# Optimization experiments

Measured on AMD Instinct MI355X. Metric: run time of the kernel, lower is better.

Reference implementation:

```python
import jax, jax.numpy as jnp
import numpy as np

B, L, D, H, DFF = 4, 2048, 1024, 16, 4096
DH = D // H
INF = 1e12


def setup_inputs() -> dict:
    key = jax.random.key(0)
    ks = jax.random.split(key, 20)
    s = lambda fan_in: 1.0 / np.sqrt(fan_in)
    inp = {
        'x': jax.random.normal(ks[0], (B, L, D), jnp.float32),
        'mask': jax.random.bernoulli(ks[1], 0.1, (B, 1, 1, L)),
        'wq': jax.random.normal(ks[2], (D, D), jnp.float32) * s(D),
        'bq': jnp.zeros((D,), jnp.float32),
        'wk': jax.random.normal(ks[3], (D, D), jnp.float32) * s(D),
        'bk': jnp.zeros((D,), jnp.float32),
        'wv': jax.random.normal(ks[4], (D, D), jnp.float32) * s(D),
        'bv': jnp.zeros((D,), jnp.float32),
        'wo': jax.random.normal(ks[5], (D, D), jnp.float32) * s(D),
        'bo': jnp.zeros((D,), jnp.float32),
        'w1': jax.random.normal(ks[6], (D, DFF), jnp.float32) * s(D),
        'b1': jnp.zeros((DFF,), jnp.float32),
        'w2': jax.random.normal(ks[7], (DFF, D), jnp.float32) * s(DFF),
        'b2': jnp.zeros((D,), jnp.float32),
        'g1': jnp.ones((D,), jnp.float32),
        'beta1': jnp.zeros((D,), jnp.float32),
        'g2': jnp.ones((D,), jnp.float32),
        'beta2': jnp.zeros((D,), jnp.float32),
    }
    return inp


def _layernorm(x, g, b, eps=1e-5):
    mu = jnp.mean(x, axis=-1, keepdims=True)
    var = jnp.mean(jnp.square(x - mu), axis=-1, keepdims=True)
    return (x - mu) * jax.lax.rsqrt(var + eps) * g + b


def reference(x, mask, wq, bq, wk, bk, wv, bv, wo, bo, w1, b1, w2, b2, g1, beta1, g2, beta2):
    # --- self attention ---
    def split_heads(t):  # [B,L,D] -> [B,H,L,DH]
        return t.reshape(B, L, H, DH).transpose(0, 2, 1, 3)

    Q = split_heads(x @ wq + bq)
    K = split_heads(x @ wk + bk)
    V = split_heads(x @ wv + bv)

    dots = jnp.einsum('bhqd,bhkd->bhqk', Q, K) / np.sqrt(DH)  # [B,H,L,L]
    dots = jnp.where(mask, -INF, dots)
    attn = jax.nn.softmax(dots, axis=-1)
    out = jnp.einsum('bhqk,bhkd->bhqd', attn, V)
    out = out.transpose(0, 2, 1, 3).reshape(B, L, D)
    out = out @ wo + bo

    x = _layernorm(x + out, g1, beta1)

    # --- feed forward ---
    h = jax.nn.relu(x @ w1 + b1)
    ff = h @ w2 + b2
    x = _layernorm(x + ff, g2, beta2)
    return x
```

## Files before the change

kernel.cpp:

```cpp
#include <hip/hip_runtime.h>
#include <hip/hip_bf16.h>

#define B_   4
#define L_   2048
#define D_   1024
#define H_   16
#define DH_  64
#define DFF_ 4096
#define M_   (B_ * L_)

typedef __attribute__((ext_vector_type(8))) short bf16x8;
typedef __attribute__((ext_vector_type(4))) float f32x4;

#define GLOAD16(gp, lp)                                                       \
  __builtin_amdgcn_global_load_lds(                                           \
      (const __attribute__((address_space(1))) unsigned int*)(gp),            \
      (__attribute__((address_space(3))) unsigned int*)(lp), 16, 0, 0)

#if __has_builtin(__builtin_amdgcn_exp2f)
#define EXP2F(x) __builtin_amdgcn_exp2f(x)
#else
#define EXP2F(x) exp2f(x)
#endif

__global__ void mask_mode_detect(const unsigned int* __restrict__ m,
                                 int* __restrict__ mode) {
  __shared__ int flags[2];
  if (threadIdx.x < 2) flags[threadIdx.x] = 0;
  __syncthreads();
  int nf32 = 0, n01 = 0;
  for (int i = threadIdx.x; i < 2048; i += 256) {
    unsigned w = m[i];
    if (w != 0u && w != 0x3f800000u) nf32 = 1;
    if (w > 1u) n01 = 1;
  }
  if (nf32) atomicOr(&flags[0], 1);
  if (n01)  atomicOr(&flags[1], 1);
  __syncthreads();
  if (threadIdx.x == 0)
    *mode = (!flags[0]) ? 0 : ((!flags[1]) ? 1 : 2);
}

__global__ void mask_prep(const void* __restrict__ m,
                          const int* __restrict__ mode_p,
                          float* __restrict__ out, int n) {
  int i = blockIdx.x * 256 + threadIdx.x;
  if (i >= n) return;
  int mode = *mode_p;
  bool mk;
  if (mode == 0)      mk = reinterpret_cast<const float*>(m)[i] != 0.f;
  else if (mode == 1) mk = reinterpret_cast<const int*>(m)[i] != 0;
  else                mk = reinterpret_cast<const unsigned char*>(m)[i] != 0;
  out[i] = mk ? -1e12f : 0.f;
}

__global__ void cvt_f32_bf16(const float4* __restrict__ in,
                             ushort4* __restrict__ out, int n4) {
  int i = blockIdx.x * 256 + threadIdx.x;
  if (i >= n4) return;
  float4 v = in[i];
  __hip_bfloat16 a = __float2bfloat16(v.x);
  __hip_bfloat16 b = __float2bfloat16(v.y);
  __hip_bfloat16 c = __float2bfloat16(v.z);
  __hip_bfloat16 d = __float2bfloat16(v.w);
  ushort4 o;
  o.x = *reinterpret_cast<unsigned short*>(&a);
  o.y = *reinterpret_cast<unsigned short*>(&b);
  o.z = *reinterpret_cast<unsigned short*>(&c);
  o.w = *reinterpret_cast<unsigned short*>(&d);
  out[i] = o;
}

__global__ void transpose_cvt(const float* __restrict__ W,
                              __hip_bfloat16* __restrict__ Wt, int K, int N) {
  __shared__ float t[32][33];
  const int n0 = blockIdx.x * 32, k0 = blockIdx.y * 32;
  const int tx = threadIdx.x, ty = threadIdx.y;
#pragma unroll
  for (int i = 0; i < 4; ++i)
    t[ty + i * 8][tx] = W[(size_t)(k0 + ty + i * 8) * N + n0 + tx];
  __syncthreads();
#pragma unroll
  for (int i = 0; i < 4; ++i)
    Wt[(size_t)(n0 + ty + i * 8) * K + k0 + tx] =
        __float2bfloat16(t[tx][ty + i * 8]);
}

__global__ void transpose_v(const __hip_bfloat16* __restrict__ Vin,
                            __hip_bfloat16* __restrict__ Vt) {
  __shared__ __hip_bfloat16 t[32][33];
  const int l0 = blockIdx.x * 32, d0 = blockIdx.y * 32, b = blockIdx.z;
  const int tx = threadIdx.x, ty = threadIdx.y;
#pragma unroll
  for (int i = 0; i < 4; ++i)
    t[ty + i * 8][tx] = Vin[(size_t)(b * L_ + l0 + ty + i * 8) * D_ + d0 + tx];
  __syncthreads();
#pragma unroll
  for (int i = 0; i < 4; ++i) {
    int d = d0 + ty + i * 8;
    Vt[(size_t)(b * D_ + d) * L_ + l0 + tx] = t[tx][ty + i * 8];
  }
}

#define STAGE8(matptr, stride, ldsbase, tile, kh, rowbase)                    \
  {                                                                           \
    _Pragma("unroll")                                                         \
    for (int j_ = 0; j_ < 2; ++j_) {                                          \
      const int s_ = j_ * 512 + tid;                                          \
      const int row_ = s_ >> 2;                                               \
// ... 99 lines not shown
  __builtin_amdgcn_s_barrier();

  for (int it = 0; it < nit; ++it) {
    const int kt = it * 2;
    const bool hn = (it + 1) < nit;
    PHASE8(0, 0, 0, 0, STAGE8(Ap, lda, ldsA + 49152, kt + 1, 1, bm));
    PHASE8(0, 1, 0, 0, STAGE8(Bp, ldb, ldsB + 49152, kt + 1, 1, bn));
    PHASE8(0, 0, 1, 0, if (hn) STAGE8(Ap, lda, ldsA, kt + 2, 0, bm));
    PHASE8(0, 1, 1, 1, if (hn) STAGE8(Bp, ldb, ldsB, kt + 2, 0, bn));
    PHASE8(32768, 0, 0, 0, if (hn) STAGE8(Ap, lda, ldsA + 16384, kt + 2, 1, bm));
    PHASE8(32768, 1, 0, 0, if (hn) STAGE8(Bp, ldb, ldsB + 16384, kt + 2, 1, bn));
    PHASE8(32768, 0, 1, 0, if (hn) STAGE8(Ap, lda, ldsA + 32768, kt + 3, 0, bm));
    PHASE8(32768, 1, 1, 1, if (hn) STAGE8(Bp, ldb, ldsB + 32768, kt + 3, 0, bn));
  }

#pragma unroll
  for (int ri = 0; ri < 8; ++ri) {
#pragma unroll
    for (int j = 0; j < 4; ++j) {
      const int col = bn + wn * 64 + j * 16 + r16;
      const float bv = (EP == 4) ? 0.f : bias[col];
#pragma unroll
      for (int r = 0; r < 4; ++r) {
        const int row = bm + wm * 128 + ri * 16 + hi * 4 + r;
        const float v = acc[ri][j][r] + bv;
        if (EP == 1) {
          ((__hip_bfloat16*)out)[(size_t)row * N + col] =
              __float2bfloat16(v > 0.f ? v : 0.f);
        } else if (EP == 3) {
          __hip_bfloat16* outp =
              (__hip_bfloat16*)out + (size_t)(col >> 10) * (M_ * D_);
          outp[(size_t)row * 1024 + (col & 1023)] = __float2bfloat16(v);
        } else {
          float* outp = (float*)out + (size_t)kh * ((size_t)M * N);
          outp[(size_t)row * N + col] = v;
        }
      }
    }
  }
}

template <int EP>
__global__ __launch_bounds__(256) void gemm_bt(
    const __hip_bfloat16* __restrict__ A, const __hip_bfloat16* __restrict__ Bt,
    const float* __restrict__ bias, const float* __restrict__ res,
    void* __restrict__ out, int M, int N, int K) {
  __shared__ __align__(16) char As[128 * 64];
  __shared__ __align__(16) char Bs[128 * 64];
  const int tid = threadIdx.x;
  const int lane = tid & 63;
  const int w = tid >> 6;
  const int wm = w >> 1, wn = w & 1;
  const int bm = blockIdx.x * 128;
  const int bn = blockIdx.y * 128;
  const int r16 = lane & 15;
  const int hi = lane >> 4;

  f32x4 acc[4][4];
#pragma unroll
  for (int m = 0; m < 4; ++m)
#pragma unroll
    for (int n = 0; n < 4; ++n) acc[m][n] = (f32x4){0.f, 0.f, 0.f, 0.f};

  for (int k0 = 0; k0 < K; k0 += 32) {
    __syncthreads();
#pragma unroll
    for (int c = 0; c < 2; ++c) {
      const int seg = c * 256 + tid;
// ... 11 lines not shown
    for (int m = 0; m < 4; ++m) {
      const int arow = wm * 64 + m * 16 + r16;
      af[m] = *reinterpret_cast<const bf16x8*>(
          As + arow * 64 + ((hi * 16) ^ ((arow & 3) << 4)));
    }
#pragma unroll
    for (int n = 0; n < 4; ++n) {
      const int brow = wn * 64 + n * 16 + r16;
      bfr[n] = *reinterpret_cast<const bf16x8*>(
          Bs + brow * 64 + ((hi * 16) ^ ((brow & 3) << 4)));
    }
#pragma unroll
    for (int m = 0; m < 4; ++m)
#pragma unroll
      for (int n = 0; n < 4; ++n)
        acc[m][n] = __builtin_amdgcn_mfma_f32_16x16x32_bf16(af[m], bfr[n],
                                                            acc[m][n], 0, 0, 0);
  }

  const int rg = hi * 4;
#pragma unroll
  for (int m = 0; m < 4; ++m) {
#pragma unroll
    for (int n = 0; n < 4; ++n) {
      const int col = bn + wn * 64 + n * 16 + r16;
      const float bv = bias[col];
#pragma unroll
      for (int r = 0; r < 4; ++r) {
        const int row = bm + wm * 64 + m * 16 + rg + r;
        const size_t idx = (size_t)row * N + col;
        float v = acc[m][n][r] + bv;
        if (EP == 0) {
          ((__hip_bfloat16*)out)[idx] = __float2bfloat16(v);
        } else if (EP == 1) {
          ((__hip_bfloat16*)out)[idx] = __float2bfloat16(v > 0.f ? v : 0.f);
        } else {
          ((float*)out)[idx] = v + res[idx];
        }
      }
    }
  }
}

__global__ __launch_bounds__(256) void attn_kernel(
    const __hip_bfloat16* __restrict__ Qg, const __hip_bfloat16* __restrict__ Kg,
    const __hip_bfloat16* __restrict__ VTg,
    const float* __restrict__ maskf,
    __hip_bfloat16* __restrict__ Og) {
  __shared__ __align__(16) char Kl[64 * 128];
  __shared__ __align__(16) char Vl[64 * 128];
  __shared__ __align__(16) char Pl[4][32 * 128];
  __shared__ float maskb[64];

  const int tid = threadIdx.x;
  const int lane = tid & 63;
  const int w = tid >> 6;
  const int hi = lane >> 4;
  const int r16 = lane & 15;
  const int swzk = (r16 & 7) << 4;

  const int nwg = gridDim.x;
  const int orig = blockIdx.x;
  const int swb = (orig & 7) * (nwg >> 3) + (orig >> 3);
  const int qb = swb & 15;
  const int bh = swb >> 4;
  const int b = bh >> 4;
  const int h = bh & 15;
  const int qbase = qb * 128 + w * 32;

  const float C = 0.18033688011112042f;

  bf16x8 qf[2][2];
#pragma unroll
  for (int m = 0; m < 2; ++m)
#pragma unroll
    for (int ks = 0; ks < 2; ++ks)
      qf[m][ks] = *reinterpret_cast<const bf16x8*>(
          &Qg[(size_t)(b * L_ + qbase + m * 16 + r16) * D_ + h * DH_ +
              ks * 32 + hi * 8]);

  float mrun[2] = {-1e30f, -1e30f};
  float lrun[2] = {0.f, 0.f};
  f32x4 o[2][4];
#pragma unroll
  for (int m = 0; m < 2; ++m)
#pragma unroll
    for (int nd = 0; nd < 4; ++nd) o[m][nd] = (f32x4){0.f, 0.f, 0.f, 0.f};

  char* const Plw = Pl[w];

  for (int kv0 = 0; kv0 < L_; kv0 += 64) {
    __syncthreads();
#pragma unroll
    for (int c = 0; c < 2; ++c) {
      const int seg = c * 256 + tid;
      const int row = seg >> 3;
      const int csl = (seg & 7) ^ (row & 7);
      GLOAD16(&Kg[(size_t)(b * L_ + kv0 + row) * D_ + h * DH_ + csl * 8],
              Kl + (c * 256 + w * 64) * 16);
      GLOAD16(&VTg[(size_t)(b * D_ + h * DH_ + row) * L_ + kv0 + csl * 8],
              Vl + (c * 256 + w * 64) * 16);
    }
    if (tid < 64) maskb[tid] = maskf[(size_t)b * L_ + kv0 + tid];
    __syncthreads();

    f32x4 sacc[2][4];
#pragma unroll
    for (int m = 0; m < 2; ++m)
#pragma unroll
      for (int n = 0; n < 4; ++n) sacc[m][n] = (f32x4){0.f, 0.f, 0.f, 0.f};
    __builtin_amdgcn_s_setprio(1);
#pragma unroll
    for (int n = 0; n < 4; ++n) {
      const int krow = n * 16 + r16;
#pragma unroll
      for (int ks = 0; ks < 2; ++ks) {
        const bf16x8 kf = *reinterpret_cast<const bf16x8*>(
            Kl + krow * 128 + ((ks * 64 + hi * 16) ^ swzk));
#pragma unroll
        for (int m = 0; m < 2; ++m)
          sacc[m][n] = __builtin_amdgcn_mfma_f32_16x16x32_bf16(
              kf, qf[m][ks], sacc[m][n], 0, 0, 0);
      }
    }
    __builtin_amdgcn_s_setprio(0);

#pragma unroll
    for (int m = 0; m < 2; ++m) {
      float p[4][4];
#pragma unroll
      for (int n = 0; n < 4; ++n) {
        const float4 mv =
            *reinterpret_cast<const float4*>(&maskb[n * 16 + hi * 4]);
        p[n][0] = fmaf(sacc[m][n][0], C, mv.x);
        p[n][1] = fmaf(sacc[m][n][1], C, mv.y);
        p[n][2] = fmaf(sacc[m][n][2], C, mv.z);
        p[n][3] = fmaf(sacc[m][n][3], C, mv.w);
      }
      float q0 = fmaxf(fmaxf(p[0][0], p[0][1]), fmaxf(p[0][2], p[0][3]));
      float q1 = fmaxf(fmaxf(p[1][0], p[1][1]), fmaxf(p[1][2], p[1][3]));
      float q2 = fmaxf(fmaxf(p[2][0], p[2][1]), fmaxf(p[2][2], p[2][3]));
      float q3 = fmaxf(fmaxf(p[3][0], p[3][1]), fmaxf(p[3][2], p[3][3]));
      float lm = fmaxf(fmaxf(q0, q1), fmaxf(q2, q3));
      lm = fmaxf(lm, __shfl_xor(lm, 16, 64));
      lm = fmaxf(lm, __shfl_xor(lm, 32, 64));
      if (!__all(lm <= mrun[m] + 8.f)) {
        const float mn = fmaxf(mrun[m], lm);
        const float corr = EXP2F(mrun[m] - mn);
        mrun[m] = mn;
        lrun[m] *= corr;
        float crs[4];
#pragma unroll
        for (int r = 0; r < 4; ++r)
          crs[r] = __shfl(corr, (lane & 48) | (hi * 4 + r), 64);
#pragma unroll
        for (int nd = 0; nd < 4; ++nd)
#pragma unroll
          for (int r = 0; r < 4; ++r) o[m][nd][r] *= crs[r];
      }
      const float mr = mrun[m];
      float ls = 0.f;
      const int prow = m * 16 + r16;
#pragma unroll
      for (int n = 0; n < 4; ++n) {
        union { unsigned long long u; unsigned short us[4]; } pk;
#pragma unroll
        for (int r = 0; r < 4; ++r) {
          const float e = EXP2F(p[n][r] - mr);
          ls += e;
          __hip_bfloat16 t = __float2bfloat16(e);
          pk.us[r] = *reinterpret_cast<unsigned short*>(&t);
        }
        *reinterpret_cast<unsigned long long*>(
            Plw + prow * 128 + ((n * 32 + hi * 8) ^ swzk)) = pk.u;
      }
      lrun[m] += ls;
    }

    bf16x8 pa[2][2];
#pragma unroll
    for (int m = 0; m < 2; ++m)
#pragma unroll
      for (int ks = 0; ks < 2; ++ks)
        pa[m][ks] = *reinterpret_cast<const bf16x8*>(
            Plw + (m * 16 + r16) * 128 + ((ks * 64 + hi * 16) ^ swzk));
    __builtin_amdgcn_s_setprio(1);
#pragma unroll
    for (int nd = 0; nd < 4; ++nd) {
      const int vrow = nd * 16 + r16;
#pragma unroll
      for (int ks = 0; ks < 2; ++ks) {
        const bf16x8 vb = *reinterpret_cast<const bf16x8*>(
            Vl + vrow * 128 + ((ks * 64 + hi * 16) ^ swzk));
#pragma unroll
        for (int m = 0; m < 2; ++m)
          o[m][nd] = __builtin_amdgcn_mfma_f32_16x16x32_bf16(pa[m][ks], vb,
                                                             o[m][nd], 0, 0, 0);
      }
    }
    __builtin_amdgcn_s_setprio(0);
  }

#pragma unroll
  for (int m = 0; m < 2; ++m) {
    lrun[m] += __shfl_xor(lrun[m], 16, 64);
    lrun[m] += __shfl_xor(lrun[m], 32, 64);
    const float inv = 1.f / lrun[m];
    float invr[4];
#pragma unroll
    for (int r = 0; r < 4; ++r)
      invr[r] = __shfl(inv, (lane & 48) | (hi * 4 + r), 64);
#pragma unroll
    for (int r = 0; r < 4; ++r) {
      const int q = qbase + m * 16 + hi * 4 + r;
#pragma unroll
      for (int nd = 0; nd < 4; ++nd)
        Og[(size_t)(b * L_ + q) * D_ + h * DH_ + nd * 16 + r16] =
            __float2bfloat16(o[m][nd][r] * invr[r]);
    }
  }
}

__global__ __launch_bounds__(256) void layernorm_kernel(
    const float* __restrict__ in, const float* __restrict__ g,
    const float* __restrict__ be, float* __restrict__ outf,
    __hip_bfloat16* __restrict__ outb) {
  const int row = blockIdx.x;
  const int tid = threadIdx.x;
  const float4 v = reinterpret_cast<const float4*>(in + (size_t)row * D_)[tid];
  float s = v.x + v.y + v.z + v.w;
  float ss = v.x * v.x + v.y * v.y + v.z * v.z + v.w * v.w;
#pragma unroll
  for (int off = 1; off < 64; off <<= 1) {
    s += __shfl_xor(s, off, 64);
    ss += __shfl_xor(ss, off, 64);
  }
  __shared__ float red[8];
  const int w = tid >> 6, lane = tid & 63;
  if (lane == 0) { red[w] = s; red[4 + w] = ss; }
  __syncthreads();
  s = red[0] + red[1] + red[2] + red[3];
  ss = red[4] + red[5] + red[6] + red[7];
  const float mu = s * (1.f / D_);
  const float rs = rsqrtf(ss * (1.f / D_) - mu * mu + 1e-5f);
  const float4 gv = reinterpret_cast<const float4*>(g)[tid];
  const float4 bv = reinterpret_cast<const float4*>(be)[tid];
  float4 ov;
  ov.x = (v.x - mu) * rs * gv.x + bv.x;
  ov.y = (v.y - mu) * rs * gv.y + bv.y;
  ov.z = (v.z - mu) * rs * gv.z + bv.z;
  ov.w = (v.w - mu) * rs * gv.w + bv.w;
  reinterpret_cast<float4*>(outf + (size_t)row * D_)[tid] = ov;
  if (outb) {
    __hip_bfloat16 t[4] = {__float2bfloat16(ov.x), __float2bfloat16(ov.y),
                           __float2bfloat16(ov.z), __float2bfloat16(ov.w)};
    *reinterpret_cast<uint2*>(&outb[(size_t)row * D_ + tid * 4]) =
        *reinterpret_cast<const uint2*>(t);
  }
}

__global__ __launch_bounds__(256) void combine_ln2(
    const float* __restrict__ P0, const float* __restrict__ P1,
    const float* __restrict__ res, const float* __restrict__ b2,
    const float* __restrict__ g, const float* __restrict__ be,
    float* __restrict__ out) {
  const int row = blockIdx.x;
  const int tid = threadIdx.x;
  const float4 a = reinterpret_cast<const float4*>(P0 + (size_t)row * D_)[tid];
  const float4 b = reinterpret_cast<const float4*>(P1 + (size_t)row * D_)[tid];
  const float4 rr = reinterpret_cast<const float4*>(res + (size_t)row * D_)[tid];
  const float4 bb = reinterpret_cast<const float4*>(b2)[tid];
  float4 v;
  v.x = a.x + b.x + rr.x + bb.x;
  v.y = a.y + b.y + rr.y + bb.y;
  v.z = a.z + b.z + rr.z + bb.z;
  v.w = a.w + b.w + rr.w + bb.w;
  float s = v.x + v.y + v.z + v.w;
  float ss = v.x * v.x + v.y * v.y + v.z * v.z + v.w * v.w;
#pragma unroll
  for (int off = 1; off < 64; off <<= 1) {
    s += __shfl_xor(s, off, 64);
    ss += __shfl_xor(ss, off, 64);
  }
  __shared__ float red[8];
  const int w = tid >> 6, lane = tid & 63;
  if (lane == 0) { red[w] = s; red[4 + w] = ss; }
  __syncthreads();
  s = red[0] + red[1] + red[2] + red[3];
  ss = red[4] + red[5] + red[6] + red[7];
  const float mu = s * (1.f / D_);
  const float rs = rsqrtf(ss * (1.f / D_) - mu * mu + 1e-5f);
  const float4 gv = reinterpret_cast<const float4*>(g)[tid];
  const float4 bv = reinterpret_cast<const float4*>(be)[tid];
  float4 ov;
  ov.x = (v.x - mu) * rs * gv.x + bv.x;
  ov.y = (v.y - mu) * rs * gv.y + bv.y;
  ov.z = (v.z - mu) * rs * gv.z + bv.z;
  ov.w = (v.w - mu) * rs * gv.w + bv.w;
  reinterpret_cast<float4*>(out + (size_t)row * D_)[tid] = ov;
}

extern "C" void kernel_launch(void* const* d_in, const int* in_sizes, int n_in,
                              void* d_out, int out_size, void* d_ws,
                              size_t ws_size, hipStream_t stream) {
  (void)in_sizes; (void)n_in; (void)out_size;
  const float* x   = (const float*)d_in[0];
  const void*  msk = d_in[1];
  const float* wq  = (const float*)d_in[2];
  const float* bq  = (const float*)d_in[3];
  const float* wk  = (const float*)d_in[4];
  const float* bk  = (const float*)d_in[5];
  const float* wv  = (const float*)d_in[6];
  const float* bv  = (const float*)d_in[7];
  const float* wo  = (const float*)d_in[8];
  const float* bo  = (const float*)d_in[9];
  const float* w1  = (const float*)d_in[10];
  const float* b1  = (const float*)d_in[11];
  const float* w2  = (const float*)d_in[12];
  const float* b2  = (const float*)d_in[13];
  const float* g1  = (const float*)d_in[14];
  const float* be1 = (const float*)d_in[15];
  const float* g2  = (const float*)d_in[16];
  const float* be2 = (const float*)d_in[17];

  char* ws = (char*)d_ws;
  int*            MODE  = (int*)(ws + 0);
  float*          MASKF = (float*)(ws + 256);
  float*          BIASC = (float*)(ws + 40960);
  __hip_bfloat16* XB    = (__hip_bfloat16*)(ws + 65536);
  __hip_bfloat16* WQT   = (__hip_bfloat16*)(ws + 16842752);
  __hip_bfloat16* WKT   = (__hip_bfloat16*)(ws + 18939904);
  __hip_bfloat16* WVT   = (__hip_bfloat16*)(ws + 21037056);
  __hip_bfloat16* WOT   = (__hip_bfloat16*)(ws + 23134208);
  __hip_bfloat16* W1T   = (__hip_bfloat16*)(ws + 25231360);
  __hip_bfloat16* W2T   = (__hip_bfloat16*)(ws + 33619968);
  __hip_bfloat16* QB    = (__hip_bfloat16*)(ws + 42008576);
  __hip_bfloat16* KB    = (__hip_bfloat16*)(ws + 58785792);
  __hip_bfloat16* VB    = (__hip_bfloat16*)(ws + 75563008);
  __hip_bfloat16* OB    = (__hip_bfloat16*)(ws + 92340224);
  __hip_bfloat16* HB    = QB;
  __hip_bfloat16* VT    = (__hip_bfloat16*)(ws + 109117440);
  float*          R1    = (float*)(ws + 125894656);
  float*          P0    = (float*)(ws + 159449088);
  float*          P1    = (float*)(ws + 193003520);
  float*          OUT   = (float*)d_out;
  const bool use_splitk = ws_size >= 226557952ull;

  mask_mode_detect<<<1, 256, 0, stream>>>((const unsigned int*)msk, MODE);
  mask_prep<<<(B_ * L_ + 255) / 256, 256, 0, stream>>>(msk, MODE, MASKF, B_ * L_);
  cvt_f32_bf16<<<(M_ * D_ / 4 + 255) / 256, 256, 0, stream>>>(
      (const float4*)x, (ushort4*)XB, M_ * D_ / 4);
  hipMemcpyAsync(BIASC, bq, D_ * 4, hipMemcpyDeviceToDevice, stream);
  hipMemcpyAsync(BIASC + D_, bk, D_ * 4, hipMemcpyDeviceToDevice, stream);
  hipMemcpyAsync(BIASC + 2 * D_, bv, D_ * 4, hipMemcpyDeviceToDevice, stream);

  dim3 tb(32, 8);
  transpose_cvt<<<dim3(D_ / 32, D_ / 32), tb, 0, stream>>>(wq, WQT, D_, D_);
  transpose_cvt<<<dim3(D_ / 32, D_ / 32), tb, 0, stream>>>(wk, WKT, D_, D_);
  transpose_cvt<<<dim3(D_ / 32, D_ / 32), tb, 0, stream>>>(wv, WVT, D_, D_);
  transpose_cvt<<<dim3(D_ / 32, D_ / 32), tb, 0, stream>>>(wo, WOT, D_, D_);
  transpose_cvt<<<dim3(DFF_ / 32, D_ / 32), tb, 0, stream>>>(w1, W1T, D_, DFF_);
  transpose_cvt<<<dim3(D_ / 32, DFF_ / 32), tb, 0, stream>>>(w2, W2T, DFF_, D_);

  gemm8<3><<<dim3((M_ / 256) * (3 * D_ / 256)), 512, 0, stream>>>(
      XB, WQT, BIASC, QB, M_, 3 * D_, D_, D_, D_);

  transpose_v<<<dim3(L_ / 32, D_ / 32, B_), tb, 0, stream>>>(VB, VT);
  attn_kernel<<<dim3(B_ * H_ * (L_ / 128)), 256, 0, stream>>>(QB, KB, VT, MASKF, OB);

  gemm_bt<2><<<dim3(M_ / 128, D_ / 128), 256, 0, stream>>>(OB, WOT, bo, x, R1, M_, D_, D_);
  layernorm_kernel<<<M_, 256, 0, stream>>>(R1, g1, be1, R1, XB);
  gemm8<1><<<dim3((M_ / 256) * (DFF_ / 256)), 512, 0, stream>>>(
      XB, W1T, b1, HB, M_, DFF_, D_, D_, D_);
  if (use_splitk) {
    gemm8<4><<<dim3((M_ / 256) * (D_ / 256) * 2), 512, 0, stream>>>(
        HB, W2T, nullptr, P0, M_, D_, DFF_ / 2, DFF_, DFF_);
    combine_ln2<<<M_, 256, 0, stream>>>(P0, P1, R1, b2, g2, be2, OUT);
  } else {
    gemm_bt<2><<<dim3(M_ / 128, D_ / 128), 256, 0, stream>>>(HB, W2T, b2, R1, OUT, M_, D_, DFF_);
    layernorm_kernel<<<M_, 256, 0, stream>>>(OUT, g2, be2, OUT, nullptr);
  }
}
```

Baseline: 474.3 us.

## Prefetch next K/V tiles in attention loop and store split-K partials as bf16

The attention kernel now issues the global-to-LDS loads for the next K tile after the QK MFMAs, and for the next V tile after the PV MFMAs. It double-buffers the mask and uses vmcnt waits with explicit barriers, so memory latency overlaps with compute instead of stalling at the top of each iteration. Separately, the split-K FFN2 partial sums are written as bf16 instead of fp32, and combine_ln2 reads them back as bf16. This halves the partial-buffer traffic and workspace size but adds rounding error to the pre-layernorm sum.

```diff
diff --git a/kernel.cpp b/kernel.cpp
--- a/kernel.cpp
+++ b/kernel.cpp
@@ -22,6 +22,10 @@
 #else
 #define EXP2F(x) exp2f(x)
 #endif
+
+__device__ __forceinline__ float bf2f(unsigned short u) {
+  return __uint_as_float(((unsigned)u) << 16);
+}
 
 __global__ void mask_mode_detect(const unsigned int* __restrict__ m,
                                  int* __restrict__ mode) {
@@ -240,8 +244,9 @@
               (__hip_bfloat16*)out + (size_t)(col >> 10) * (M_ * D_);
           outp[(size_t)row * 1024 + (col & 1023)] = __float2bfloat16(v);
         } else {
-          float* outp = (float*)out + (size_t)kh * ((size_t)M * N);
-          outp[(size_t)row * N + col] = v;
+          __hip_bfloat16* outp =
+              (__hip_bfloat16*)out + (size_t)kh * ((size_t)M * N);
+          outp[(size_t)row * N + col] = __float2bfloat16(v);
         }
       }
     }
@@ -337,7 +342,7 @@
   __shared__ __align__(16) char Kl[64 * 128];
   __shared__ __align__(16) char Vl[64 * 128];
   __shared__ __align__(16) char Pl[4][32 * 128];
-  __shared__ float maskb[64];
+  __shared__ float maskb[2][64];
 
   const int tid = threadIdx.x;
   const int lane = tid & 63;
@@ -357,6 +362,27 @@
 
   const float C = 0.18033688011112042f;
 
+#define STAGE_K(kvv)                                                          \
+  {                                                                           \
+    _Pragma("unroll") for (int c_ = 0; c_ < 2; ++c_) {                        \
+      const int seg_ = c_ * 256 + tid;                                        \
+      const int row_ = seg_ >> 3;                                             \
+      const int csl_ = (seg_ & 7) ^ (row_ & 7);                               \
+      GLOAD16(&Kg[(size_t)(b * L_ + (kvv) + row_) * D_ + h * DH_ + csl_ * 8], \
+              Kl + (c_ * 256 + w * 64) * 16);                                 \
+    }                                                                         \
+  }
+#define STAGE_V(kvv)                                                          \
+  {                                                                           \
+    _Pragma("unroll") for (int c_ = 0; c_ < 2; ++c_) {                        \
+      const int seg_ = c_ * 256 + tid;                                        \
+      const int row_ = seg_ >> 3;                                             \
+      const int csl_ = (seg_ & 7) ^ (row_ & 7);                               \
+      GLOAD16(&VTg[(size_t)(b * D_ + h * DH_ + row_) * L_ + (kvv) + csl_ * 8],\
+              Vl + (c_ * 256 + w * 64) * 16);                                 \
+    }                                                                         \
+  }
+
   bf16x8 qf[2][2];
 #pragma unroll
   for (int m = 0; m < 2; ++m)
@@ -376,20 +402,19 @@
 
   char* const Plw = Pl[w];
 
-  for (int kv0 = 0; kv0 < L_; kv0 += 64) {
-    __syncthreads();
-#pragma unroll
-    for (int c = 0; c < 2; ++c) {
-      const int seg = c * 256 + tid;
-      const int row = seg >> 3;
-      const int csl = (seg & 7) ^ (row & 7);
-      GLOAD16(&Kg[(size_t)(b * L_ + kv0 + row) * D_ + h * DH_ + csl * 8],
-              Kl + (c * 256 + w * 64) * 16);
-      GLOAD16(&VTg[(size_t)(b * D_ + h * DH_ + row) * L_ + kv0 + csl * 8],
-              Vl + (c * 256 + w * 64) * 16);
-    }
-    if (tid < 64) maskb[tid] = maskf[(size_t)b * L_ + kv0 + tid];
-    __syncthreads();
+  STAGE_K(0);
+  float mreg = 0.f;
+  if (tid < 64) mreg = maskf[(size_t)b * L_ + tid];
+  STAGE_V(0);
+  if (tid < 64) maskb[0][tid] = mreg;
+  asm volatile("s_waitcnt vmcnt(2)" ::: "memory");
+  __builtin_amdgcn_sched_barrier(0);
+  __builtin_amdgcn_s_barrier();
+  __builtin_amdgcn_sched_barrier(0);
+
+  for (int t = 0; t < 32; ++t) {
+    const int slot = t & 1;
+    const int kvn = ((t + 1) & 31) * 64;
 
     f32x4 sacc[2][4];
 #pragma unroll
@@ -411,6 +436,9 @@
       }
     }
     __builtin_amdgcn_s_setprio(0);
+    __builtin_amdgcn_s_barrier();
+    __builtin_amdgcn_sched_barrier(0);
+    STAGE_K(kvn);
 
 #pragma unroll
     for (int m = 0; m < 2; ++m) {
@@ -418,7 +446,7 @@
 #pragma unroll
       for (int n = 0; n < 4; ++n) {
         const float4 mv =
-            *reinterpret_cast<const float4*>(&maskb[n * 16 + hi * 4]);
+            *reinterpret_cast<const float4*>(&maskb[slot][n * 16 + hi * 4]);
         p[n][0] = fmaf(sacc[m][n][0], C, mv.x);
         p[n][1] = fmaf(sacc[m][n][1], C, mv.y);
         p[n][2] = fmaf(sacc[m][n][2], C, mv.z);
@@ -455,8 +483,8 @@
         for (int r = 0; r < 4; ++r) {
           const float e = EXP2F(p[n][r] - mr);
           ls += e;
-          __hip_bfloat16 t = __float2bfloat16(e);
-          pk.us[r] = *reinterpret_cast<unsigned short*>(&t);
+          __hip_bfloat16 tt = __float2bfloat16(e);
+          pk.us[r] = *reinterpret_cast<unsigned short*>(&tt);
         }
         *reinterpret_cast<unsigned long long*>(
             Plw + prow * 128 + ((n * 32 + hi * 8) ^ swzk)) = pk.u;
@@ -464,6 +492,11 @@
       lrun[m] += ls;
     }
 
+    asm volatile("s_waitcnt vmcnt(2)" ::: "memory");
+    __builtin_amdgcn_sched_barrier(0);
+    __builtin_amdgcn_s_barrier();
+    __builtin_amdgcn_sched_barrier(0);
+
     bf16x8 pa[2][2];
 #pragma unroll
     for (int m = 0; m < 2; ++m)
@@ -486,6 +519,16 @@
       }
     }
     __builtin_amdgcn_s_setprio(0);
+    __builtin_amdgcn_s_barrier();
+    __builtin_amdgcn_sched_barrier(0);
+
+    if (tid < 64) mreg = maskf[(size_t)b * L_ + kvn + tid];
+    STAGE_V(kvn);
+    if (tid < 64) maskb[slot ^ 1][tid] = mreg;
+    asm volatile("s_waitcnt vmcnt(2)" ::: "memory");
+    __builtin_amdgcn_sched_barrier(0);
+    __builtin_amdgcn_s_barrier();
+    __builtin_amdgcn_sched_barrier(0);
   }
 
 #pragma unroll
@@ -506,6 +549,8 @@
             __float2bfloat16(o[m][nd][r] * invr[r]);
     }
   }
+#undef STAGE_K
+#undef STAGE_V
 }
 
 __global__ __launch_bounds__(256) void layernorm_kernel(
@@ -547,21 +592,23 @@
 }
 
 __global__ __launch_bounds__(256) void combine_ln2(
-    const float* __restrict__ P0, const float* __restrict__ P1,
+    const __hip_bfloat16* __restrict__ P0, const __hip_bfloat16* __restrict__ P1,
     const float* __restrict__ res, const float* __restrict__ b2,
     const float* __restrict__ g, const float* __restrict__ be,
     float* __restrict__ out) {
   const int row = blockIdx.x;
   const int tid = threadIdx.x;
-  const float4 a = reinterpret_cast<const float4*>(P0 + (size_t)row * D_)[tid];
-  const float4 b = reinterpret_cast<const float4*>(P1 + (size_t)row * D_)[tid];
+  const ushort4 a4 =
+      reinterpret_cast<const ushort4*>(P0 + (size_t)row * D_)[tid];
+  const ushort4 b4 =
+      reinterpret_cast<const ushort4*>(P1 + (size_t)row * D_)[tid];
   const float4 rr = reinterpret_cast<const float4*>(res + (size_t)row * D_)[tid];
   const float4 bb = reinterpret_cast<const float4*>(b2)[tid];
   float4 v;
-  v.x = a.x + b.x + rr.x + bb.x;
-  v.y = a.y + b.y + rr.y + bb.y;
-  v.z = a.z + b.z + rr.z + bb.z;
-  v.w = a.w + b.w + rr.w + bb.w;
+  v.x = bf2f(a4.x) + bf2f(b4.x) + rr.x + bb.x;
+  v.y = bf2f(a4.y) + bf2f(b4.y) + rr.y + bb.y;
+  v.z = bf2f(a4.z) + bf2f(b4.z) + rr.z + bb.z;
+  v.w = bf2f(a4.w) + bf2f(b4.w) + rr.w + bb.w;
   float s = v.x + v.y + v.z + v.w;
   float ss = v.x * v.x + v.y * v.y + v.z * v.z + v.w * v.w;
 #pragma unroll
@@ -628,10 +675,10 @@
   __hip_bfloat16* HB    = QB;
   __hip_bfloat16* VT    = (__hip_bfloat16*)(ws + 109117440);
   float*          R1    = (float*)(ws + 125894656);
-  float*          P0    = (float*)(ws + 159449088);
-  float*          P1    = (float*)(ws + 193003520);
+  __hip_bfloat16* P0    = (__hip_bfloat16*)(ws + 159449088);
+  __hip_bfloat16* P1    = (__hip_bfloat16*)(ws + 176226304);
   float*          OUT   = (float*)d_out;
-  const bool use_splitk = ws_size >= 226557952ull;
+  const bool use_splitk = ws_size >= 193003520ull;
 
   mask_mode_detect<<<1, 256, 0, stream>>>((const unsigned int*)msk, MODE);
   mask_prep<<<(B_ * L_ + 255) / 256, 256, 0, stream>>>(msk, MODE, MASKF, B_ * L_);
```

Result: faster. 463.6 us (-2.3%).

## Use 32x32 MFMA with register-resident P in attention; bf16 split-K partials

Applied to the files above, without the earlier changes.

The attention kernel moves from 16x16x32 to 32x32x16 bf16 MFMA tiles with one 32-row query block per wave. The softmax probabilities are packed to bf16 in registers and exchanged across half-waves with shuffles instead of a round trip through per-wave LDS, which removes the P shared buffer. Separately, the split-K FFN2 partials are stored as bf16 rather than fp32 and the combine/LayerNorm kernel reads bf16, halving that traffic at some precision cost. The workspace threshold for enabling split-K is lowered to match the smaller buffers.

```diff
diff --git a/kernel.cpp b/kernel.cpp
--- a/kernel.cpp
+++ b/kernel.cpp
@@ -11,6 +11,7 @@
 
 typedef __attribute__((ext_vector_type(8))) short bf16x8;
 typedef __attribute__((ext_vector_type(4))) float f32x4;
+typedef __attribute__((ext_vector_type(16))) float f32x16;
 
 #define GLOAD16(gp, lp)                                                       \
   __builtin_amdgcn_global_load_lds(                                           \
@@ -22,6 +23,15 @@
 #else
 #define EXP2F(x) exp2f(x)
 #endif
+
+__device__ __forceinline__ float bf2f(unsigned short u) {
+  return __uint_as_float(((unsigned)u) << 16);
+}
+__device__ __forceinline__ unsigned cvt_pk_bf16(float lo, float hi) {
+  unsigned r;
+  asm("v_cvt_pk_bf16_f32 %0, %1, %2" : "=v"(r) : "v"(lo), "v"(hi));
+  return r;
+}
 
 __global__ void mask_mode_detect(const unsigned int* __restrict__ m,
                                  int* __restrict__ mode) {
@@ -240,8 +250,9 @@
               (__hip_bfloat16*)out + (size_t)(col >> 10) * (M_ * D_);
           outp[(size_t)row * 1024 + (col & 1023)] = __float2bfloat16(v);
         } else {
-          float* outp = (float*)out + (size_t)kh * ((size_t)M * N);
-          outp[(size_t)row * N + col] = v;
+          __hip_bfloat16* outp =
+              (__hip_bfloat16*)out + (size_t)kh * ((size_t)M * N);
+          outp[(size_t)row * N + col] = __float2bfloat16(v);
         }
       }
     }
@@ -336,15 +347,13 @@
     __hip_bfloat16* __restrict__ Og) {
   __shared__ __align__(16) char Kl[64 * 128];
   __shared__ __align__(16) char Vl[64 * 128];
-  __shared__ __align__(16) char Pl[4][32 * 128];
   __shared__ float maskb[64];
 
   const int tid = threadIdx.x;
   const int lane = tid & 63;
   const int w = tid >> 6;
-  const int hi = lane >> 4;
-  const int r16 = lane & 15;
-  const int swzk = (r16 & 7) << 4;
+  const int l31 = lane & 31;
+  const int h5 = lane >> 5;
 
   const int nwg = gridDim.x;
   const int orig = blockIdx.x;
@@ -357,24 +366,19 @@
 
   const float C = 0.18033688011112042f;
 
-  bf16x8 qf[2][2];
-#pragma unroll
-  for (int m = 0; m < 2; ++m)
-#pragma unroll
-    for (int ks = 0; ks < 2; ++ks)
-      qf[m][ks] = *reinterpret_cast<const bf16x8*>(
-          &Qg[(size_t)(b * L_ + qbase + m * 16 + r16) * D_ + h * DH_ +
-              ks * 32 + hi * 8]);
-
-  float mrun[2] = {-1e30f, -1e30f};
-  float lrun[2] = {0.f, 0.f};
-  f32x4 o[2][4];
-#pragma unroll
-  for (int m = 0; m < 2; ++m)
-#pragma unroll
-    for (int nd = 0; nd < 4; ++nd) o[m][nd] = (f32x4){0.f, 0.f, 0.f, 0.f};
-
-  char* const Plw = Pl[w];
+  bf16x8 qf[4];
+#pragma unroll
+  for (int dk = 0; dk < 4; ++dk)
+    qf[dk] = *reinterpret_cast<const bf16x8*>(
+        &Qg[(size_t)(b * L_ + qbase + l31) * D_ + h * DH_ + dk * 16 + h5 * 8]);
+
+  float mrun = -1e30f;
+  float lrun = 0.f;
+  f32x16 o[2];
+#pragma unroll
+  for (int nd = 0; nd < 2; ++nd)
+#pragma unroll
+    for (int r = 0; r < 16; ++r) o[nd][r] = 0.f;
 
   for (int kv0 = 0; kv0 < L_; kv0 += 64) {
     __syncthreads();
@@ -391,120 +395,122 @@
     if (tid < 64) maskb[tid] = maskf[(size_t)b * L_ + kv0 + tid];
     __syncthreads();
 
-    f32x4 sacc[2][4];
-#pragma unroll
-    for (int m = 0; m < 2; ++m)
-#pragma unroll
-      for (int n = 0; n < 4; ++n) sacc[m][n] = (f32x4){0.f, 0.f, 0.f, 0.f};
+    f32x16 sac[2];
+#pragma unroll
+    for (int n = 0; n < 2; ++n)
+#pragma unroll
+      for (int r = 0; r < 16; ++r) sac[n][r] = 0.f;
     __builtin_amdgcn_s_setprio(1);
 #pragma unroll
-    for (int n = 0; n < 4; ++n) {
-      const int krow = n * 16 + r16;
-#pragma unroll
-      for (int ks = 0; ks < 2; ++ks) {
+    for (int n = 0; n < 2; ++n) {
+      const int krow = n * 32 + l31;
+      const int rsw = (krow & 7) << 4;
+#pragma unroll
+      for (int dk = 0; dk < 4; ++dk) {
         const bf16x8 kf = *reinterpret_cast<const bf16x8*>(
-            Kl + krow * 128 + ((ks * 64 + hi * 16) ^ swzk));
-#pragma unroll
-        for (int m = 0; m < 2; ++m)
-          sacc[m][n] = __builtin_amdgcn_mfma_f32_16x16x32_bf16(
-              kf, qf[m][ks], sacc[m][n], 0, 0, 0);
+            Kl + krow * 128 + ((dk * 32 + h5 * 16) ^ rsw));
+        sac[n] = __builtin_amdgcn_mfma_f32_32x32x16_bf16(kf, qf[dk], sac[n],
+                                                         0, 0, 0);
       }
     }
     __builtin_amdgcn_s_setprio(0);
 
 #pragma unroll
-    for (int m = 0; m < 2; ++m) {
-      float p[4][4];
-#pragma unroll
-      for (int n = 0; n < 4; ++n) {
-        const float4 mv =
-            *reinterpret_cast<const float4*>(&maskb[n * 16 + hi * 4]);
-        p[n][0] = fmaf(sacc[m][n][0], C, mv.x);
-        p[n][1] = fmaf(sacc[m][n][1], C, mv.y);
-        p[n][2] = fmaf(sacc[m][n][2], C, mv.z);
-        p[n][3] = fmaf(sacc[m][n][3], C, mv.w);
+    for (int n = 0; n < 2; ++n)
+#pragma unroll
+      for (int q_ = 0; q_ < 4; ++q_) {
+        const float4 mv = *reinterpret_cast<const float4*>(
+            &maskb[n * 32 + q_ * 8 + h5 * 4]);
+        sac[n][q_ * 4 + 0] = fmaf(sac[n][q_ * 4 + 0], C, mv.x);
+        sac[n][q_ * 4 + 1] = fmaf(sac[n][q_ * 4 + 1], C, mv.y);
+        sac[n][q_ * 4 + 2] = fmaf(sac[n][q_ * 4 + 2], C, mv.z);
+        sac[n][q_ * 4 + 3] = fmaf(sac[n][q_ * 4 + 3], C, mv.w);
       }
-      float q0 = fmaxf(fmaxf(p[0][0], p[0][1]), fmaxf(p[0][2], p[0][3]));
-      float q1 = fmaxf(fmaxf(p[1][0], p[1][1]), fmaxf(p[1][2], p[1][3]));
-      float q2 = fmaxf(fmaxf(p[2][0], p[2][1]), fmaxf(p[2][2], p[2][3]));
-      float q3 = fmaxf(fmaxf(p[3][0], p[3][1]), fmaxf(p[3][2], p[3][3]));
-      float lm = fmaxf(fmaxf(q0, q1), fmaxf(q2, q3));
-      lm = fmaxf(lm, __shfl_xor(lm, 16, 64));
-      lm = fmaxf(lm, __shfl_xor(lm, 32, 64));
-      if (!__all(lm <= mrun[m] + 8.f)) {
-        const float mn = fmaxf(mrun[m], lm);
-        const float corr = EXP2F(mrun[m] - mn);
-        mrun[m] = mn;
-        lrun[m] *= corr;
-        float crs[4];
-#pragma unroll
-        for (int r = 0; r < 4; ++r)
-          crs[r] = __shfl(corr, (lane & 48) | (hi * 4 + r), 64);
-#pragma unroll
-        for (int nd = 0; nd < 4; ++nd)
-#pragma unroll
-          for (int r = 0; r < 4; ++r) o[m][nd][r] *= crs[r];
+
+    float lm = sac[0][0];
+#pragma unroll
+    for (int n = 0; n < 2; ++n)
+#pragma unroll
+      for (int r = 0; r < 16; ++r) lm = fmaxf(lm, sac[n][r]);
+    lm = fmaxf(lm, __shfl_xor(lm, 32, 64));
+
+    if (!__all(lm <= mrun + 8.f)) {
+      const float mn = fmaxf(mrun, lm);
+      const float corr = EXP2F(mrun - mn);
+      mrun = mn;
+      lrun *= corr;
+#pragma unroll
+      for (int r = 0; r < 16; ++r) {
+        const int ql = (r & 3) + 8 * (r >> 2) + 4 * h5;
+        const float cr = __shfl(corr, ql, 64);
+        o[0][r] *= cr;
+        o[1][r] *= cr;
       }
-      const float mr = mrun[m];
-      float ls = 0.f;
-      const int prow = m * 16 + r16;
-#pragma unroll
-      for (int n = 0; n < 4; ++n) {
-        union { unsigned long long u; unsigned short us[4]; } pk;
-#pragma unroll
-        for (int r = 0; r < 4; ++r) {
-          const float e = EXP2F(p[n][r] - mr);
-          ls += e;
-          __hip_bfloat16 t = __float2bfloat16(e);
-          pk.us[r] = *reinterpret_cast<unsigned short*>(&t);
-        }
-        *reinterpret_cast<unsigned long long*>(
-            Plw + prow * 128 + ((n * 32 + hi * 8) ^ swzk)) = pk.u;
+    }
+
+    const float mr = mrun;
+    float ls = 0.f;
+    unsigned pp[2][4][2];
+#pragma unroll
+    for (int n = 0; n < 2; ++n)
+#pragma unroll
+      for (int q_ = 0; q_ < 4; ++q_) {
+        float e0 = EXP2F(sac[n][q_ * 4 + 0] - mr);
+        float e1 = EXP2F(sac[n][q_ * 4 + 1] - mr);
+        float e2 = EXP2F(sac[n][q_ * 4 + 2] - mr);
+        float e3 = EXP2F(sac[n][q_ * 4 + 3] - mr);
+        ls += (e0 + e1) + (e2 + e3);
+        pp[n][q_][0] = cvt_pk_bf16(e0, e1);
+        pp[n][q_][1] = cvt_pk_bf16(e2, e3);
       }
-      lrun[m] += ls;
-    }
-
-    bf16x8 pa[2][2];
-#pragma unroll
-    for (int m = 0; m < 2; ++m)
-#pragma unroll
-      for (int ks = 0; ks < 2; ++ks)
-        pa[m][ks] = *reinterpret_cast<const bf16x8*>(
-            Plw + (m * 16 + r16) * 128 + ((ks * 64 + hi * 16) ^ swzk));
+    lrun += ls;
+
+    bf16x8 pa[4];
+#pragma unroll
+    for (int kb = 0; kb < 4; ++kb) {
+      const int n = kb >> 1;
+      const int qe = (kb & 1) * 2;
+      const unsigned oe0 = pp[n][qe][0], oe1 = pp[n][qe][1];
+      const unsigned oo0 = pp[n][qe + 1][0], oo1 = pp[n][qe + 1][1];
+      const unsigned xe0 = __shfl_xor(oe0, 32, 64);
+      const unsigned xe1 = __shfl_xor(oe1, 32, 64);
+      const unsigned xo0 = __shfl_xor(oo0, 32, 64);
+      const unsigned xo1 = __shfl_xor(oo1, 32, 64);
+      union { unsigned u[4]; bf16x8 v; } pu;
+      pu.u[0] = h5 ? xo0 : oe0;
+      pu.u[1] = h5 ? xo1 : oe1;
+      pu.u[2] = h5 ? oo0 : xe0;
+      pu.u[3] = h5 ? oo1 : xe1;
+      pa[kb] = pu.v;
+    }
+
     __builtin_amdgcn_s_setprio(1);
 #pragma unroll
-    for (int nd = 0; nd < 4; ++nd) {
-      const int vrow = nd * 16 + r16;
-#pragma unroll
-      for (int ks = 0; ks < 2; ++ks) {
+    for (int nd = 0; nd < 2; ++nd) {
+      const int vrow = nd * 32 + l31;
+      const int rsw = (vrow & 7) << 4;
+#pragma unroll
+      for (int kb = 0; kb < 4; ++kb) {
         const bf16x8 vb = *reinterpret_cast<const bf16x8*>(
-            Vl + vrow * 128 + ((ks * 64 + hi * 16) ^ swzk));
-#pragma unroll
-        for (int m = 0; m < 2; ++m)
-          o[m][nd] = __builtin_amdgcn_mfma_f32_16x16x32_bf16(pa[m][ks], vb,
-                                                             o[m][nd], 0, 0, 0);
+            Vl + vrow * 128 + ((kb * 32 + h5 * 16) ^ rsw));
+        o[nd] = __builtin_amdgcn_mfma_f32_32x32x16_bf16(pa[kb], vb, o[nd],
+                                                        0, 0, 0);
       }
     }
     __builtin_amdgcn_s_setprio(0);
   }
 
-#pragma unroll
-  for (int m = 0; m < 2; ++m) {
-    lrun[m] += __shfl_xor(lrun[m], 16, 64);
-    lrun[m] += __shfl_xor(lrun[m], 32, 64);
-    const float inv = 1.f / lrun[m];
-    float invr[4];
-#pragma unroll
-    for (int r = 0; r < 4; ++r)
-      invr[r] = __shfl(inv, (lane & 48) | (hi * 4 + r), 64);
-#pragma unroll
-    for (int r = 0; r < 4; ++r) {
-      const int q = qbase + m * 16 + hi * 4 + r;
-#pragma unroll
-      for (int nd = 0; nd < 4; ++nd)
-        Og[(size_t)(b * L_ + q) * D_ + h * DH_ + nd * 16 + r16] =
-            __float2bfloat16(o[m][nd][r] * invr[r]);
-    }
+  lrun += __shfl_xor(lrun, 32, 64);
+  const float inv = 1.f / lrun;
+#pragma unroll
+  for (int r = 0; r < 16; ++r) {
+    const int ql = (r & 3) + 8 * (r >> 2) + 4 * h5;
+    const float ir = __shfl(inv, ql, 64);
+    const int q = qbase + ql;
+#pragma unroll
+    for (int nd = 0; nd < 2; ++nd)
+      Og[(size_t)(b * L_ + q) * D_ + h * DH_ + nd * 32 + l31] =
+          __float2bfloat16(o[nd][r] * ir);
   }
 }
 
@@ -547,21 +553,23 @@
 }
 
 __global__ __launch_bounds__(256) void combine_ln2(
-    const float* __restrict__ P0, const float* __restrict__ P1,
+    const __hip_bfloat16* __restrict__ P0, const __hip_bfloat16* __restrict__ P1,
     const float* __restrict__ res, const float* __restrict__ b2,
     const float* __restrict__ g, const float* __restrict__ be,
     float* __restrict__ out) {
   const int row = blockIdx.x;
   const int tid = threadIdx.x;
-  const float4 a = reinterpret_cast<const float4*>(P0 + (size_t)row * D_)[tid];
-  const float4 b = reinterpret_cast<const float4*>(P1 + (size_t)row * D_)[tid];
+  const ushort4 a4 =
+      reinterpret_cast<const ushort4*>(P0 + (size_t)row * D_)[tid];
+  const ushort4 b4 =
+      reinterpret_cast<const ushort4*>(P1 + (size_t)row * D_)[tid];
   const float4 rr = reinterpret_cast<const float4*>(res + (size_t)row * D_)[tid];
   const float4 bb = reinterpret_cast<const float4*>(b2)[tid];
   float4 v;
-  v.x = a.x + b.x + rr.x + bb.x;
-  v.y = a.y + b.y + rr.y + bb.y;
-  v.z = a.z + b.z + rr.z + bb.z;
-  v.w = a.w + b.w + rr.w + bb.w;
+  v.x = bf2f(a4.x) + bf2f(b4.x) + rr.x + bb.x;
+  v.y = bf2f(a4.y) + bf2f(b4.y) + rr.y + bb.y;
+  v.z = bf2f(a4.z) + bf2f(b4.z) + rr.z + bb.z;
+  v.w = bf2f(a4.w) + bf2f(b4.w) + rr.w + bb.w;
   float s = v.x + v.y + v.z + v.w;
   float ss = v.x * v.x + v.y * v.y + v.z * v.z + v.w * v.w;
 #pragma unroll
@@ -628,10 +636,10 @@
   __hip_bfloat16* HB    = QB;
   __hip_bfloat16* VT    = (__hip_bfloat16*)(ws + 109117440);
   float*          R1    = (float*)(ws + 125894656);
-  float*          P0    = (float*)(ws + 159449088);
-  float*          P1    = (float*)(ws + 193003520);
+  __hip_bfloat16* P0    = (__hip_bfloat16*)(ws + 159449088);
+  __hip_bfloat16* P1    = (__hip_bfloat16*)(ws + 176226304);
   float*          OUT   = (float*)d_out;
-  const bool use_splitk = ws_size >= 226557952ull;
+  const bool use_splitk = ws_size >= 193003520ull;
 
   mask_mode_detect<<<1, 256, 0, stream>>>((const unsigned int*)msk, MODE);
   mask_prep<<<(B_ * L_ + 255) / 256, 256, 0, stream>>>(msk, MODE, MASKF, B_ * L_);
```

New measurement: 467.7 us. No clear change (-1.4%).

## Merge prep kernels, batch weight transposes, and store GEMM partials in bf16

Applied to the files above, without the earlier changes.

Mask-mode detection, mask preparation and bias concatenation now run in one kernel, and the six weight transpose launches become a single launch. The output projection now writes bf16 with no residual, and the residual add moves into a new layernorm kernel. The split-K FFN2 partials are stored as bf16 instead of fp32. This cuts launch count and global memory traffic, at the cost of extra rounding error in the partial sums and projection output.

```diff
diff --git a/kernel.cpp b/kernel.cpp
--- a/kernel.cpp
+++ b/kernel.cpp
@@ -23,35 +23,46 @@
 #define EXP2F(x) exp2f(x)
 #endif
 
-__global__ void mask_mode_detect(const unsigned int* __restrict__ m,
-                                 int* __restrict__ mode) {
+__device__ __forceinline__ float bf2f(unsigned short u) {
+  return __uint_as_float(((unsigned)u) << 16);
+}
+
+__global__ void prep_kernel(const unsigned int* __restrict__ mraw,
+                            float* __restrict__ maskf,
+                            const float* __restrict__ bq,
+                            const float* __restrict__ bk,
+                            const float* __restrict__ bv,
+                            float* __restrict__ biasc) {
   __shared__ int flags[2];
   if (threadIdx.x < 2) flags[threadIdx.x] = 0;
   __syncthreads();
   int nf32 = 0, n01 = 0;
   for (int i = threadIdx.x; i < 2048; i += 256) {
-    unsigned w = m[i];
+    unsigned w = mraw[i];
     if (w != 0u && w != 0x3f800000u) nf32 = 1;
     if (w > 1u) n01 = 1;
   }
   if (nf32) atomicOr(&flags[0], 1);
   if (n01)  atomicOr(&flags[1], 1);
   __syncthreads();
-  if (threadIdx.x == 0)
-    *mode = (!flags[0]) ? 0 : ((!flags[1]) ? 1 : 2);
-}
-
-__global__ void mask_prep(const void* __restrict__ m,
-                          const int* __restrict__ mode_p,
-                          float* __restrict__ out, int n) {
-  int i = blockIdx.x * 256 + threadIdx.x;
-  if (i >= n) return;
-  int mode = *mode_p;
-  bool mk;
-  if (mode == 0)      mk = reinterpret_cast<const float*>(m)[i] != 0.f;
-  else if (mode == 1) mk = reinterpret_cast<const int*>(m)[i] != 0;
-  else                mk = reinterpret_cast<const unsigned char*>(m)[i] != 0;
-  out[i] = mk ? -1e12f : 0.f;
+  const int mode = (!flags[0]) ? 0 : ((!flags[1]) ? 1 : 2);
+  const int i = blockIdx.x * 256 + threadIdx.x;
+  if (i < B_ * L_) {
+    bool mk;
+    if (mode == 0)      mk = reinterpret_cast<const float*>(mraw)[i] != 0.f;
+    else if (mode == 1) mk = reinterpret_cast<const int*>(mraw)[i] != 0;
+    else                mk = reinterpret_cast<const unsigned char*>(mraw)[i] != 0;
+    maskf[i] = mk ? -1e12f : 0.f;
+  }
+  if (blockIdx.x == 0) {
+#pragma unroll
+    for (int j = 0; j < 4; ++j) {
+      const int c = j * 256 + threadIdx.x;
+      biasc[c] = bq[c];
+      biasc[D_ + c] = bk[c];
+      biasc[2 * D_ + c] = bv[c];
+    }
+  }
 }
 
 __global__ void cvt_f32_bf16(const float4* __restrict__ in,
@@ -71,10 +82,30 @@
   out[i] = o;
 }
 
-__global__ void transpose_cvt(const float* __restrict__ W,
-                              __hip_bfloat16* __restrict__ Wt, int K, int N) {
+__global__ void transpose_cvt_all(
+    const float* __restrict__ wq, const float* __restrict__ wk,
+    const float* __restrict__ wv, const float* __restrict__ wo,
+    const float* __restrict__ w1, const float* __restrict__ w2,
+    __hip_bfloat16* __restrict__ WQT, __hip_bfloat16* __restrict__ WKT,
+    __hip_bfloat16* __restrict__ WVT, __hip_bfloat16* __restrict__ WOT,
+    __hip_bfloat16* __restrict__ W1T, __hip_bfloat16* __restrict__ W2T) {
   __shared__ float t[32][33];
-  const int n0 = blockIdx.x * 32, k0 = blockIdx.y * 32;
+  const int id = blockIdx.x;
+  const float* W;
+  __hip_bfloat16* Wt;
+  int K, N, rem;
+  if (id < 4096) {
+    const int which = id >> 10;
+    W  = which == 0 ? wq : which == 1 ? wk : which == 2 ? wv : wo;
+    Wt = which == 0 ? WQT : which == 1 ? WKT : which == 2 ? WVT : WOT;
+    K = D_; N = D_; rem = id & 1023;
+  } else if (id < 8192) {
+    W = w1; Wt = W1T; K = D_; N = DFF_; rem = id - 4096;
+  } else {
+    W = w2; Wt = W2T; K = DFF_; N = D_; rem = id - 8192;
+  }
+  const int ntx = N >> 5;
+  const int n0 = (rem % ntx) * 32, k0 = (rem / ntx) * 32;
   const int tx = threadIdx.x, ty = threadIdx.y;
 #pragma unroll
   for (int i = 0; i < 4; ++i)
@@ -240,8 +271,9 @@
               (__hip_bfloat16*)out + (size_t)(col >> 10) * (M_ * D_);
           outp[(size_t)row * 1024 + (col & 1023)] = __float2bfloat16(v);
         } else {
-          float* outp = (float*)out + (size_t)kh * ((size_t)M * N);
-          outp[(size_t)row * N + col] = v;
+          __hip_bfloat16* outp =
+              (__hip_bfloat16*)out + (size_t)kh * ((size_t)M * N);
+          outp[(size_t)row * N + col] = __float2bfloat16(v);
         }
       }
     }
@@ -319,8 +351,6 @@
         float v = acc[m][n][r] + bv;
         if (EP == 0) {
           ((__hip_bfloat16*)out)[idx] = __float2bfloat16(v);
-        } else if (EP == 1) {
-          ((__hip_bfloat16*)out)[idx] = __float2bfloat16(v > 0.f ? v : 0.f);
         } else {
           ((float*)out)[idx] = v + res[idx];
         }
@@ -546,22 +576,66 @@
   }
 }
 
+__global__ __launch_bounds__(256) void ln_addres(
+    const __hip_bfloat16* __restrict__ OP, const float* __restrict__ x,
+    const float* __restrict__ g, const float* __restrict__ be,
+    float* __restrict__ outf, __hip_bfloat16* __restrict__ outb) {
+  const int row = blockIdx.x;
+  const int tid = threadIdx.x;
+  const ushort4 a4 = reinterpret_cast<const ushort4*>(OP + (size_t)row * D_)[tid];
+  const float4 xr = reinterpret_cast<const float4*>(x + (size_t)row * D_)[tid];
+  float4 v;
+  v.x = bf2f(a4.x) + xr.x;
+  v.y = bf2f(a4.y) + xr.y;
+  v.z = bf2f(a4.z) + xr.z;
+  v.w = bf2f(a4.w) + xr.w;
+  float s = v.x + v.y + v.z + v.w;
+  float ss = v.x * v.x + v.y * v.y + v.z * v.z + v.w * v.w;
+#pragma unroll
+  for (int off = 1; off < 64; off <<= 1) {
+    s += __shfl_xor(s, off, 64);
+    ss += __shfl_xor(ss, off, 64);
+  }
+  __shared__ float red[8];
+  const int w = tid >> 6, lane = tid & 63;
+  if (lane == 0) { red[w] = s; red[4 + w] = ss; }
+  __syncthreads();
+  s = red[0] + red[1] + red[2] + red[3];
+  ss = red[4] + red[5] + red[6] + red[7];
+  const float mu = s * (1.f / D_);
+  const float rs = rsqrtf(ss * (1.f / D_) - mu * mu + 1e-5f);
+  const float4 gv = reinterpret_cast<const float4*>(g)[tid];
+  const float4 bv = reinterpret_cast<const float4*>(be)[tid];
+  float4 ov;
+  ov.x = (v.x - mu) * rs * gv.x + bv.x;
+  ov.y = (v.y - mu) * rs * gv.y + bv.y;
+  ov.z = (v.z - mu) * rs * gv.z + bv.z;
+  ov.w = (v.w - mu) * rs * gv.w + bv.w;
+  reinterpret_cast<float4*>(outf + (size_t)row * D_)[tid] = ov;
+  __hip_bfloat16 t[4] = {__float2bfloat16(ov.x), __float2bfloat16(ov.y),
+                         __float2bfloat16(ov.z), __float2bfloat16(ov.w)};
+  *reinterpret_cast<uint2*>(&outb[(size_t)row * D_ + tid * 4]) =
+      *reinterpret_cast<const uint2*>(t);
+}
+
 __global__ __launch_bounds__(256) void combine_ln2(
-    const float* __restrict__ P0, const float* __restrict__ P1,
+    const __hip_bfloat16* __restrict__ P0, const __hip_bfloat16* __restrict__ P1,
     const float* __restrict__ res, const float* __restrict__ b2,
     const float* __restrict__ g, const float* __restrict__ be,
     float* __restrict__ out) {
   const int row = blockIdx.x;
   const int tid = threadIdx.x;
-  const float4 a = reinterpret_cast<const float4*>(P0 + (size_t)row * D_)[tid];
-  const float4 b = reinterpret_cast<const float4*>(P1 + (size_t)row * D_)[tid];
+  const ushort4 a4 =
+      reinterpret_cast<const ushort4*>(P0 + (size_t)row * D_)[tid];
+  const ushort4 b4 =
+      reinterpret_cast<const ushort4*>(P1 + (size_t)row * D_)[tid];
   const float4 rr = reinterpret_cast<const float4*>(res + (size_t)row * D_)[tid];
   const float4 bb = reinterpret_cast<const float4*>(b2)[tid];
   float4 v;
-  v.x = a.x + b.x + rr.x + bb.x;
-  v.y = a.y + b.y + rr.y + bb.y;
-  v.z = a.z + b.z + rr.z + bb.z;
-  v.w = a.w + b.w + rr.w + bb.w;
+  v.x = bf2f(a4.x) + bf2f(b4.x) + rr.x + bb.x;
+  v.y = bf2f(a4.y) + bf2f(b4.y) + rr.y + bb.y;
+  v.z = bf2f(a4.z) + bf2f(b4.z) + rr.z + bb.z;
+  v.w = bf2f(a4.w) + bf2f(b4.w) + rr.w + bb.w;
   float s = v.x + v.y + v.z + v.w;
   float ss = v.x * v.x + v.y * v.y + v.z * v.z + v.w * v.w;
 #pragma unroll
@@ -611,7 +685,6 @@
   const float* be2 = (const float*)d_in[17];
 
   char* ws = (char*)d_ws;
-  int*            MODE  = (int*)(ws + 0);
   float*          MASKF = (float*)(ws + 256);
   float*          BIASC = (float*)(ws + 40960);
   __hip_bfloat16* XB    = (__hip_bfloat16*)(ws + 65536);
@@ -627,36 +700,29 @@
   __hip_bfloat16* OB    = (__hip_bfloat16*)(ws + 92340224);
   __hip_bfloat16* HB    = QB;
   __hip_bfloat16* VT    = (__hip_bfloat16*)(ws + 109117440);
+  __hip_bfloat16* OP    = VT;
   float*          R1    = (float*)(ws + 125894656);
-  float*          P0    = (float*)(ws + 159449088);
-  float*          P1    = (float*)(ws + 193003520);
+  __hip_bfloat16* P0    = (__hip_bfloat16*)(ws + 159449088);
+  __hip_bfloat16* P1    = (__hip_bfloat16*)(ws + 176226304);
   float*          OUT   = (float*)d_out;
-  const bool use_splitk = ws_size >= 226557952ull;
-
-  mask_mode_detect<<<1, 256, 0, stream>>>((const unsigned int*)msk, MODE);
-  mask_prep<<<(B_ * L_ + 255) / 256, 256, 0, stream>>>(msk, MODE, MASKF, B_ * L_);
+  const bool use_splitk = ws_size >= 193003520ull;
+
+  prep_kernel<<<(B_ * L_ + 255) / 256, 256, 0, stream>>>(
+      (const unsigned int*)msk, MASKF, bq, bk, bv, BIASC);
   cvt_f32_bf16<<<(M_ * D_ / 4 + 255) / 256, 256, 0, stream>>>(
       (const float4*)x, (ushort4*)XB, M_ * D_ / 4);
-  hipMemcpyAsync(BIASC, bq, D_ * 4, hipMemcpyDeviceToDevice, stream);
-  hipMemcpyAsync(BIASC + D_, bk, D_ * 4, hipMemcpyDeviceToDevice, stream);
-  hipMemcpyAsync(BIASC + 2 * D_, bv, D_ * 4, hipMemcpyDeviceToDevice, stream);
-
-  dim3 tb(32, 8);
-  transpose_cvt<<<dim3(D_ / 32, D_ / 32), tb, 0, stream>>>(wq, WQT, D_, D_);
-  transpose_cvt<<<dim3(D_ / 32, D_ / 32), tb, 0, stream>>>(wk, WKT, D_, D_);
-  transpose_cvt<<<dim3(D_ / 32, D_ / 32), tb, 0, stream>>>(wv, WVT, D_, D_);
-  transpose_cvt<<<dim3(D_ / 32, D_ / 32), tb, 0, stream>>>(wo, WOT, D_, D_);
-  transpose_cvt<<<dim3(DFF_ / 32, D_ / 32), tb, 0, stream>>>(w1, W1T, D_, DFF_);
-  transpose_cvt<<<dim3(D_ / 32, DFF_ / 32), tb, 0, stream>>>(w2, W2T, DFF_, D_);
+  transpose_cvt_all<<<12288, dim3(32, 8), 0, stream>>>(
+      wq, wk, wv, wo, w1, w2, WQT, WKT, WVT, WOT, W1T, W2T);
 
   gemm8<3><<<dim3((M_ / 256) * (3 * D_ / 256)), 512, 0, stream>>>(
       XB, WQT, BIASC, QB, M_, 3 * D_, D_, D_, D_);
 
-  transpose_v<<<dim3(L_ / 32, D_ / 32, B_), tb, 0, stream>>>(VB, VT);
+  transpose_v<<<dim3(L_ / 32, D_ / 32, B_), dim3(32, 8), 0, stream>>>(VB, VT);
   attn_kernel<<<dim3(B_ * H_ * (L_ / 128)), 256, 0, stream>>>(QB, KB, VT, MASKF, OB);
 
-  gemm_bt<2><<<dim3(M_ / 128, D_ / 128), 256, 0, stream>>>(OB, WOT, bo, x, R1, M_, D_, D_);
-  layernorm_kernel<<<M_, 256, 0, stream>>>(R1, g1, be1, R1, XB);
+  gemm_bt<0><<<dim3(M_ / 128, D_ / 128), 256, 0, stream>>>(OB, WOT, bo, nullptr, OP, M_, D_, D_);
+  ln_addres<<<M_, 256, 0, stream>>>(OP, x, g1, be1, R1, XB);
+
   gemm8<1><<<dim3((M_ / 256) * (DFF_ / 256)), 512, 0, stream>>>(
       XB, W1T, b1, HB, M_, DFF_, D_, D_, D_);
   if (use_splitk) {
```

Result: faster. 441.4 us (-6.9%).
